# Kernel optimization log

Hardware: AMD Instinct MI355X
Metric: run time of the kernel (lower is better)

## Reference

```python
import jax, jax.numpy as jnp
import numpy as np

BS, HS, NH = 8, 3, 8          # block_size, halo_size, num_heads
WIN = BS + 2 * HS             # 14
DQK = 16                      # dim_head_qk = make_divisible(128*1.0)//8
DV = 16                       # dim_head_v = 128 // 8
SCALE = DQK ** -0.5


def _rel_pos_index():
    # Faithful numpy port of QueryFreePosEmbedRel._get_relative_position_index
    w = WIN
    coords = np.stack(np.meshgrid(np.arange(w), np.arange(w), indexing='ij'))  # (2,w,w)
    flat = coords.reshape(2, -1)                                               # (2, w*w)
    rel = flat[:, :, None] - flat[:, None, :]                                  # (2, ww, ww)
    rel = rel.transpose(1, 2, 0).astype(np.int64)
    rel[:, :, 0] += w - 1
    rel[:, :, 1] += w - 1
    rel[:, :, 0] *= 2 * w - 1
    rel = rel.sum(-1).reshape(w, w, w, w)
    sh = (w - BS) // 2  # == halo_size
    rel = rel[sh:sh + BS, sh:sh + BS, :, :].reshape(BS * BS, w * w)
    return rel

_REL_IDX = _rel_pos_index()


def setup_inputs() -> dict:
    key = jax.random.key(0)
    k1, k2, k3, k4, k5, k6 = jax.random.split(key, 6)
    C = 128
    dim_out_qk = NH * DQK   # 128
    dim_out_v = NH * DV     # 128
    x = jax.random.normal(k1, (4, 128, 128, C), dtype=jnp.float32)
    q_w = jax.random.normal(k2, (dim_out_qk, C), dtype=jnp.float32) * 0.05
    kv_w = jax.random.normal(k3, (dim_out_qk + dim_out_v, C), dtype=jnp.float32) * 0.05
    pos_table = jax.random.normal(k4, ((2 * WIN - 1) * (2 * WIN - 1), NH), dtype=jnp.float32) * 0.02
    proj_w = jax.random.normal(k5, (dim_out_v, dim_out_v), dtype=jnp.float32) * 0.05
    proj_b = jax.random.normal(k6, (dim_out_v,), dtype=jnp.float32) * 0.01
    return {"x": x, "q_w": q_w, "kv_w": kv_w, "pos_table": pos_table,
            "proj_w": proj_w, "proj_b": proj_b}


def reference(x, q_w, kv_w, pos_table, proj_w, proj_b):
    B, H, W, C = x.shape  # H,W divisible by BS -> no padding branch
    nhb, nwb = H // BS, W // BS
    nb = nhb * nwb

    # --- queries: (B,NH,nb,bs^2,DQK), block-partitioned ---
    q = x @ q_w.T
    q = q.reshape(B, nhb, BS, nwb, BS, NH, DQK).transpose(0, 5, 1, 3, 2, 4, 6)
    q = q.reshape(B, NH, nb, BS * BS, DQK)

    # --- kv 1x1 conv + halo padding + overlapping window extraction ---
    kv = x @ kv_w.T                                   # (B,H,W, NH*(DQK+DV))
    kv = jnp.pad(kv, ((0, 0), (HS, HS), (HS, HS), (0, 0)))
    ri = (np.arange(nhb) * BS)[:, None] + np.arange(WIN)[None, :]
    ci = (np.arange(nwb) * BS)[:, None] + np.arange(WIN)[None, :]
    kvw = kv[:, ri]
    kvw = kvw[:, :, :, ci]
    kvw = kvw.transpose(0, 1, 3, 2, 4, 5).reshape(B, nb, WIN * WIN, NH, DQK + DV)
    kvw = kvw.transpose(0, 3, 1, 2, 4)
    k = kvw[..., :DQK]
    v = kvw[..., DQK:]

    bias = pos_table[_REL_IDX.reshape(-1)].reshape(BS * BS, WIN * WIN, NH)
    bias = bias.transpose(2, 0, 1)[None, :, None]

    # --- scores + halo-boundary mask + softmax ---
    attn = jnp.einsum('bhnqd,bhnkd->bhnqk', q * SCALE, k) + bias
    ones = jnp.pad(jnp.ones((H, W), jnp.float32), ((HS, HS), (HS, HS)))
    mw = ones[ri][:, :, ci].transpose(0, 2, 1, 3).reshape(nb, WIN * WIN)
    valid = (mw > 0)[None, None, :, None, :]
    attn = jnp.where(valid, attn, -jnp.finfo(attn.dtype).max)
    attn = jax.nn.softmax(attn, axis=-1)

    # --- weighted sum over V, fold blocks back to (B,H,W,dim_out_v) ---
    out = jnp.einsum('bhnqk,bhnkd->bhnqd', attn, v)   # (B,NH,nb,bs^2,DV)
    out = out.reshape(B, NH, nhb, nwb, BS, BS, DV)
    out = out.transpose(0, 2, 4, 3, 5, 1, 6).reshape(B, H, W, NH * DV)
    return out @ proj_w.T + proj_b
```

## Files before the change

kernel.cpp:

```cpp
#include <hip/hip_runtime.h>
#include <float.h>


typedef float f32x4 __attribute__((ext_vector_type(4)));
typedef short s16x4 __attribute__((ext_vector_type(4)));
typedef short s16x8 __attribute__((ext_vector_type(8)));
typedef unsigned int u32x2 __attribute__((ext_vector_type(2)));
typedef unsigned int u32x4 __attribute__((ext_vector_type(4)));

__device__ inline ushort f2bf(float f) {
    unsigned u = __float_as_uint(f);
    return (ushort)((u + 0x7FFF + ((u >> 16) & 1)) >> 16);
}
__device__ inline float bf2f(ushort h) { return __uint_as_float((unsigned)h << 16); }
__device__ inline unsigned cvtpk(float a, float b) {
    unsigned r;
    asm("v_cvt_pk_bf16_f32 %0, %1, %2" : "=v"(r) : "v"(a), "v"(b));
    return r;
}
#if __has_builtin(__builtin_amdgcn_exp2f)
#define EXP2(x) __builtin_amdgcn_exp2f(x)
#else
#define EXP2(x) exp2f(x)
#endif

__global__ __launch_bounds__(256) void conv_w(
    const float* __restrict__ q_w, const float* __restrict__ kv_w,
    const float* __restrict__ proj_w, ushort* whi, ushort* wlo)
{
    const int g = blockIdx.x * 256 + threadIdx.x;
    const int row = g >> 7, col = g & 127;
    const float v = (row < 128) ? q_w[row * 128 + col]
                  : (row < 384) ? kv_w[(row - 128) * 128 + col]
                                : proj_w[(row - 384) * 128 + col];
    const ushort h = f2bf(v);
    const int off = ((row >> 4) * 2048) + ((col >> 3) * 128) + ((row & 15) * 8) + (col & 7);
    whi[off] = h;
    wlo[off] = f2bf(v - bf2f(h));
}

__global__ __launch_bounds__(256) void gemm_split(
    const float* A,
    const ushort* __restrict__ Whi, const ushort* __restrict__ Wlo,
    int wbase, int ntc, int tok1,
    ushort* qb, ushort* kvb, float* outf, const float* __restrict__ bias)
{
    __shared__ ushort Ah[128 * 128];
    __shared__ ushort Al[128 * 128];

    const int t = threadIdx.x;
    const int row0 = blockIdx.x * 128;
    const int w = t >> 6, l = t & 63;
    const int wm = w >> 1, wn = w & 1;
    const int lr = l & 15, cA = l >> 4;

#pragma unroll
    for (int i = 0; i < 16; ++i) {
        const int idx = t + i * 256;
        const int p = idx >> 5, fc = idx & 31;
        const float4 v = *(const float4*)(A + (size_t)(row0 + p) * 128 + fc * 4);
        const int base = p * 128 + (((fc >> 1) ^ (p & 7)) << 3) + (fc & 1) * 4;
        const unsigned h01 = cvtpk(v.x, v.y), h23 = cvtpk(v.z, v.w);
        *(u32x2*)&Ah[base] = (u32x2){h01, h23};
        const float hx = __uint_as_float(h01 << 16);
        const float hy = __uint_as_float(h01 & 0xFFFF0000u);
        const float hz = __uint_as_float(h23 << 16);
        const float hw = __uint_as_float(h23 & 0xFFFF0000u);
        *(u32x2*)&Al[base] = (u32x2){ cvtpk(v.x - hx, v.y - hy),
                                      cvtpk(v.z - hz, v.w - hw) };
    }
    __syncthreads();

#pragma unroll 1
    for (int nt = 0; nt < ntc; ++nt) {
        f32x4 acc[4][4];
#pragma unroll
        for (int mf = 0; mf < 4; ++mf)
#pragma unroll
            for (int nf = 0; nf < 4; ++nf) acc[mf][nf] = (f32x4){0.f,0.f,0.f,0.f};

#pragma unroll 1
        for (int kk = 0; kk < 4; ++kk) {
            s16x8 wh[4], wl[4];
#pragma unroll
            for (int nf = 0; nf < 4; ++nf) {
                const int rb = (wbase >> 4) + nt * 8 + wn * 4 + nf;
                const size_t off = (size_t)rb * 2048 + (kk * 4 + cA) * 128 + lr * 8;
                wh[nf] = *(const s16x8*)&Whi[off];
                wl[nf] = *(const s16x8*)&Wlo[off];
            }
#pragma unroll
            for (int mf = 0; mf < 4; ++mf) {
                const int p = wm * 64 + mf * 16 + lr;
                const int off = p * 128 + ((((kk << 2) + cA) ^ (p & 7)) << 3);
                const s16x8 xh = *(const s16x8*)&Ah[off];
                const s16x8 xl = *(const s16x8*)&Al[off];
#pragma unroll
                for (int nf = 0; nf < 4; ++nf) {
                    acc[mf][nf] = __builtin_amdgcn_mfma_f32_16x16x32_bf16(
                                      wh[nf], xh, acc[mf][nf], 0, 0, 0);
                    acc[mf][nf] = __builtin_amdgcn_mfma_f32_16x16x32_bf16(
                                      wh[nf], xl, acc[mf][nf], 0, 0, 0);
                    acc[mf][nf] = __builtin_amdgcn_mfma_f32_16x16x32_bf16(
                                      wl[nf], xh, acc[mf][nf], 0, 0, 0);
                }
            }
        }

#pragma unroll
        for (int mf = 0; mf < 4; ++mf) {
            const size_t pix = row0 + wm * 64 + mf * 16 + lr;
#pragma unroll
            for (int nf = 0; nf < 4; ++nf) {
                const int chan = wn * 64 + nf * 16 + cA * 4;
                const f32x4 o = acc[mf][nf];
                if (tok1) {
                    const u32x2 pk = (u32x2){ cvtpk(o[0], o[1]), cvtpk(o[2], o[3]) };
                    if (nt == 0) {
                        const int head = wn * 4 + nf;
                        *(u32x2*)(qb + ((size_t)head << 20) + pix * 16 + (chan & 15)) = pk;
                    } else {
                        const int gchan = (nt - 1) * 128 + chan;
                        const int head = gchan >> 5;
                        *(u32x2*)(kvb + ((size_t)head << 21) + pix * 32 + (gchan & 31)) = pk;
                    }
                } else {
                    const float4 bv = *(const float4*)(bias + chan);
                    f32x4 r = o;
                    r[0] += bv.x; r[1] += bv.y; r[2] += bv.z; r[3] += bv.w;
                    *(f32x4*)(outf + pix * 128 + chan) = r;
                }
            }
        }
    }
}

__global__ __launch_bounds__(256) void halo_attn(
    float* out,
    const ushort* __restrict__ qg,
    const ushort* __restrict__ kvg,
    const float* __restrict__ pos_table)
{
    __shared__ ushort VT[2][16][232];
    __shared__ float  bias_l[648];
    __shared__ int    keyoff[256];
    __shared__ short  koff2[224];

    const int t  = threadIdx.x;
    const int bi = blockIdx.x, head = blockIdx.y, bp = blockIdx.z;
    const int by = bi >> 4, bx = bi & 15;
    const int w  = t >> 6;
    const int lb = w >> 1;
    const int qh = w & 1;
    const int batch = bp * 2 + lb;
    const int l  = t & 63;
    const int lr = l & 15;
    const int cA = l >> 4;

    const char* kvh = (const char*)(kvg + ((size_t)head << 21) + ((size_t)batch << 19));

    if (t < 224) {
        const int wy = t / 14, wx = t - (t / 14) * 14;
        const int py = by * 8 + wy - 3, px = bx * 8 + wx - 3;
        const bool valid = (t < 196) && ((unsigned)py < 128u) && ((unsigned)px < 128u);
        keyoff[t] = valid ? ((py * 128 + px) * 64) : 0;
        koff2[t]  = valid ? (short)(wy * 21 + wx) : (short)(-200);
    } else {
        keyoff[t] = 0;
    }
    for (int i = t; i < 648; i += 256) {
        if (i < 441) {
            const int ry = i / 21, rx = i - ry * 21;
            bias_l[i] = pos_table[((ry + 3) * 27 + rx + 3) * 8 + head] * 1.44269504f;
        } else {
            bias_l[i] = -30000.0f;
        }
    }
    __syncthreads();

    {
        const int l2 = qh * 64 + l;
        if (l2 < 112) {
            const char* base = kvh + 32;
            const char* s0 = base + keyoff[2 * l2];
            const char* s1 = base + keyoff[2 * l2 + 1];
            const s16x8 a0 = *(const s16x8*)s0;
            const s16x8 a1 = *(const s16x8*)(s0 + 16);
            const s16x8 c0 = *(const s16x8*)s1;
            const s16x8 c1 = *(const s16x8*)(s1 + 16);
#pragma unroll
            for (int j = 0; j < 8; ++j) {
                *(unsigned*)&VT[lb][j][2 * l2] =
                    ((unsigned)(ushort)c0[j] << 16) | (ushort)a0[j];
                *(unsigned*)&VT[lb][j + 8][2 * l2] =
                    ((unsigned)(ushort)c1[j] << 16) | (ushort)a1[j];
            }
        }
    }
    __syncthreads();

    const int gbase = ((lr >> 2) << 3) + (lr & 3);
    const ushort* qhp = qg + ((size_t)head << 20);
    s16x8 qf[2];
    float* optr[2];
    int qoff2[2];
#pragma unroll
    for (int j = 0; j < 2; ++j) {
        const int q = (qh * 2 + j) * 16 + lr;
        const int qy = q >> 3, qx = q & 7;
        const size_t pix = ((size_t)(batch * 128 + by * 8 + qy)) * 128 + bx * 8 + qx;
        optr[j] = out + pix * 128 + head * 16 + cA * 4;
        qoff2[j] = (qy + 13) * 21 + (qx + 13);
#pragma unroll
        for (int k = 0; k < 8; ++k) qf[j][k] = 0;
        if (cA < 2)
            qf[j] = *(const s16x8*)(qhp + pix * 16 + cA * 8);
    }

    f32x4 accv[2];
    float sumf[2];
#pragma unroll
    for (int j = 0; j < 2; ++j) {
        accv[j] = (f32x4){0.f, 0.f, 0.f, 0.f};
        sumf[j] = 0.f;
    }

    s16x8 ak0 = *(const s16x8*)(kvh + keyoff[gbase]     + cA * 16);
    s16x8 ak1 = *(const s16x8*)(kvh + keyoff[gbase + 4] + cA * 16);

#pragma unroll 1
    for (int m = 0; m < 7; ++m) {
        const int nx = 32 * (m + 1) + gbase;
        const s16x8 nk0 = *(const s16x8*)(kvh + keyoff[nx]     + cA * 16);
        const s16x8 nk1 = *(const s16x8*)(kvh + keyoff[nx + 4] + cA * 16);

        const int kb = 32 * m + cA * 8;
        const s16x8 kk = *(const s16x8*)&koff2[kb];
        const s16x8 vt = *(const s16x8*)&VT[lb][lr][kb];

#pragma unroll
        for (int j = 0; j < 2; ++j) {
            const f32x4 sf0 = __builtin_amdgcn_mfma_f32_16x16x32_bf16(
                                  ak0, qf[j], (f32x4){0.f, 0.f, 0.f, 0.f}, 0, 0, 0);
            const f32x4 sf1 = __builtin_amdgcn_mfma_f32_16x16x32_bf16(
                                  ak1, qf[j], (f32x4){0.f, 0.f, 0.f, 0.f}, 0, 0, 0);
            float pr0[4], pr1[4];
#pragma unroll
            for (int r = 0; r < 4; ++r)
                pr0[r] = EXP2(fmaf(sf0[r], 0.36067376f, bias_l[qoff2[j] - (int)kk[r]]));
#pragma unroll
            for (int r = 0; r < 4; ++r)
                pr1[r] = EXP2(fmaf(sf1[r], 0.36067376f, bias_l[qoff2[j] - (int)kk[4 + r]]));
            sumf[j] += ((pr0[0] + pr0[1]) + (pr0[2] + pr0[3]))
                     + ((pr1[0] + pr1[1]) + (pr1[2] + pr1[3]));

            const u32x4 pk = (u32x4){ cvtpk(pr0[0], pr0[1]), cvtpk(pr0[2], pr0[3]),
                                      cvtpk(pr1[0], pr1[1]), cvtpk(pr1[2], pr1[3]) };
            const s16x8 pb = *(const s16x8*)&pk;
            accv[j] = __builtin_amdgcn_mfma_f32_16x16x32_bf16(vt, pb, accv[j], 0, 0, 0);
        }
        ak0 = nk0;
        ak1 = nk1;
    }

#pragma unroll
    for (int j = 0; j < 2; ++j) {
        float s = sumf[j];
        s += __shfl_xor(s, 16);
        s += __shfl_xor(s, 32);
        const float inv = 1.0f / s;
        *(f32x4*)optr[j] = accv[j] * inv;
    }
}

extern "C" void kernel_launch(void* const* d_in, const int* in_sizes, int n_in,
                              void* d_out, int out_size, void* d_ws, size_t ws_size,
                              hipStream_t stream) {
    const float* x      = (const float*)d_in[0];
    const float* q_w    = (const float*)d_in[1];
    const float* kv_w   = (const float*)d_in[2];
    const float* pt     = (const float*)d_in[3];
    const float* proj_w = (const float*)d_in[4];
    const float* proj_b = (const float*)d_in[5];
    float* out = (float*)d_out;

    ushort* ykvb = (ushort*)d_ws;
    ushort* qb   = (ushort*)((char*)d_ws + 33554432);
    ushort* whi  = (ushort*)((char*)d_ws + 33554432 + 16777216);
    ushort* wlo  = whi + 65536;

    const dim3 blk(256);
    conv_w<<<dim3(256), blk, 0, stream>>>(q_w, kv_w, proj_w, whi, wlo);
    gemm_split<<<dim3(512), blk, 0, stream>>>(x, whi, wlo, 0, 3, 1,
                                              qb, ykvb, nullptr, nullptr);
    halo_attn<<<dim3(256, 8, 2), blk, 0, stream>>>(out, qb, ykvb, pt);
    gemm_split<<<dim3(512), blk, 0, stream>>>(out, whi, wlo, 384, 1, 0,
                                              nullptr, nullptr, out, proj_b);
}
```

Measured before the change: 94.13 us.

## Compute softmax denominator via MFMA with validity vector and direct bias addressing

Lays out the key window with a stride of 16 instead of 14, so the relative-position bias index becomes an affine pointer that steps back each iteration. This replaces the per-key koff2 lookup and its gather. Invalid keys are no longer masked by a large negative bias. Their V rows are zeroed, and a bf16 ones/zeros validity vector goes through an extra MFMA that yields the masked softmax denominator, replacing the scalar sum and cross-lane shuffles. The cost is one more MFMA per query tile per step, plus exp values that are computed but thrown away for invalid keys; bf16-rounded probabilities in the denominator may also shift accuracy slightly.

```diff
diff --git a/kernel.cpp b/kernel.cpp
--- a/kernel.cpp
+++ b/kernel.cpp
@@ -142,17 +142,17 @@
     const float* __restrict__ pos_table)
 {
     __shared__ ushort VT[2][16][232];
-    __shared__ float  bias_l[648];
+    __shared__ float  bias_l[444];
     __shared__ int    keyoff[256];
-    __shared__ short  koff2[224];
+    __shared__ ushort vbf[232];
 
     const int t  = threadIdx.x;
-    const int bi = blockIdx.x, head = blockIdx.y, bp = blockIdx.z;
+    const int bi = blockIdx.x, head = blockIdx.y, bpair = blockIdx.z;
     const int by = bi >> 4, bx = bi & 15;
     const int w  = t >> 6;
     const int lb = w >> 1;
     const int qh = w & 1;
-    const int batch = bp * 2 + lb;
+    const int batch = bpair * 2 + lb;
     const int l  = t & 63;
     const int lr = l & 15;
     const int cA = l >> 4;
@@ -160,21 +160,22 @@
     const char* kvh = (const char*)(kvg + ((size_t)head << 21) + ((size_t)batch << 19));
 
     if (t < 224) {
-        const int wy = t / 14, wx = t - (t / 14) * 14;
+        const int wy = t >> 4, wx = t & 15;
         const int py = by * 8 + wy - 3, px = bx * 8 + wx - 3;
-        const bool valid = (t < 196) && ((unsigned)py < 128u) && ((unsigned)px < 128u);
+        const bool valid = (wx < 14) && ((unsigned)py < 128u) && ((unsigned)px < 128u);
         keyoff[t] = valid ? ((py * 128 + px) * 64) : 0;
-        koff2[t]  = valid ? (short)(wy * 21 + wx) : (short)(-200);
+        vbf[t]    = valid ? (ushort)0x3F80 : (ushort)0;
     } else {
         keyoff[t] = 0;
-    }
-    for (int i = t; i < 648; i += 256) {
-        if (i < 441) {
-            const int ry = i / 21, rx = i - ry * 21;
-            bias_l[i] = pos_table[((ry + 3) * 27 + rx + 3) * 8 + head] * 1.44269504f;
-        } else {
-            bias_l[i] = -30000.0f;
-        }
+        if (t < 232) vbf[t] = 0;
+    }
+    for (int i = t; i < 444; i += 256) {
+        float v = 0.f;
+        if (i >= 2) {
+            const int r = i - 2, ry = r / 21, rx = r - ry * 21;
+            v = pos_table[((ry + 3) * 27 + rx + 3) * 8 + head] * 1.44269504f;
+        }
+        bias_l[i] = v;
     }
     __syncthreads();
 
@@ -182,12 +183,15 @@
         const int l2 = qh * 64 + l;
         if (l2 < 112) {
             const char* base = kvh + 32;
+            const bool v0 = vbf[2 * l2] != 0;
+            const bool v1 = vbf[2 * l2 + 1] != 0;
+            const s16x8 z = (s16x8){0,0,0,0,0,0,0,0};
             const char* s0 = base + keyoff[2 * l2];
             const char* s1 = base + keyoff[2 * l2 + 1];
-            const s16x8 a0 = *(const s16x8*)s0;
-            const s16x8 a1 = *(const s16x8*)(s0 + 16);
-            const s16x8 c0 = *(const s16x8*)s1;
-            const s16x8 c1 = *(const s16x8*)(s1 + 16);
+            const s16x8 a0 = v0 ? *(const s16x8*)s0 : z;
+            const s16x8 a1 = v0 ? *(const s16x8*)(s0 + 16) : z;
+            const s16x8 c0 = v1 ? *(const s16x8*)s1 : z;
+            const s16x8 c1 = v1 ? *(const s16x8*)(s1 + 16) : z;
 #pragma unroll
             for (int j = 0; j < 8; ++j) {
                 *(unsigned*)&VT[lb][j][2 * l2] =
@@ -201,28 +205,28 @@
 
     const int gbase = ((lr >> 2) << 3) + (lr & 3);
     const ushort* qhp = qg + ((size_t)head << 20);
+    const int wy0 = cA >> 1, wx0 = (cA & 1) * 8;
     s16x8 qf[2];
     float* optr[2];
-    int qoff2[2];
+    const float* bptr[2];
 #pragma unroll
     for (int j = 0; j < 2; ++j) {
         const int q = (qh * 2 + j) * 16 + lr;
         const int qy = q >> 3, qx = q & 7;
         const size_t pix = ((size_t)(batch * 128 + by * 8 + qy)) * 128 + bx * 8 + qx;
         optr[j] = out + pix * 128 + head * 16 + cA * 4;
-        qoff2[j] = (qy + 13) * 21 + (qx + 13);
+        bptr[j] = bias_l + 2 + (qy + 13 - wy0) * 21 + (qx + 6 - wx0);
 #pragma unroll
         for (int k = 0; k < 8; ++k) qf[j][k] = 0;
         if (cA < 2)
             qf[j] = *(const s16x8*)(qhp + pix * 16 + cA * 8);
     }
 
-    f32x4 accv[2];
-    float sumf[2];
+    f32x4 accv[2], accs[2];
 #pragma unroll
     for (int j = 0; j < 2; ++j) {
         accv[j] = (f32x4){0.f, 0.f, 0.f, 0.f};
-        sumf[j] = 0.f;
+        accs[j] = (f32x4){0.f, 0.f, 0.f, 0.f};
     }
 
     s16x8 ak0 = *(const s16x8*)(kvh + keyoff[gbase]     + cA * 16);
@@ -235,8 +239,8 @@
         const s16x8 nk1 = *(const s16x8*)(kvh + keyoff[nx + 4] + cA * 16);
 
         const int kb = 32 * m + cA * 8;
-        const s16x8 kk = *(const s16x8*)&koff2[kb];
-        const s16x8 vt = *(const s16x8*)&VT[lb][lr][kb];
+        const s16x8 vt  = *(const s16x8*)&VT[lb][lr][kb];
+        const s16x8 vld = *(const s16x8*)&vbf[kb];
 
 #pragma unroll
         for (int j = 0; j < 2; ++j) {
@@ -244,31 +248,30 @@
                                   ak0, qf[j], (f32x4){0.f, 0.f, 0.f, 0.f}, 0, 0, 0);
             const f32x4 sf1 = __builtin_amdgcn_mfma_f32_16x16x32_bf16(
                                   ak1, qf[j], (f32x4){0.f, 0.f, 0.f, 0.f}, 0, 0, 0);
+            const float* bq = bptr[j];
             float pr0[4], pr1[4];
 #pragma unroll
             for (int r = 0; r < 4; ++r)
-                pr0[r] = EXP2(fmaf(sf0[r], 0.36067376f, bias_l[qoff2[j] - (int)kk[r]]));
+                pr0[r] = EXP2(fmaf(sf0[r], 0.36067376f, bq[7 - r]));
 #pragma unroll
             for (int r = 0; r < 4; ++r)
-                pr1[r] = EXP2(fmaf(sf1[r], 0.36067376f, bias_l[qoff2[j] - (int)kk[4 + r]]));
-            sumf[j] += ((pr0[0] + pr0[1]) + (pr0[2] + pr0[3]))
-                     + ((pr1[0] + pr1[1]) + (pr1[2] + pr1[3]));
+                pr1[r] = EXP2(fmaf(sf1[r], 0.36067376f, bq[3 - r]));
 
             const u32x4 pk = (u32x4){ cvtpk(pr0[0], pr0[1]), cvtpk(pr0[2], pr0[3]),
                                       cvtpk(pr1[0], pr1[1]), cvtpk(pr1[2], pr1[3]) };
             const s16x8 pb = *(const s16x8*)&pk;
-            accv[j] = __builtin_amdgcn_mfma_f32_16x16x32_bf16(vt, pb, accv[j], 0, 0, 0);
-        }
+            accv[j] = __builtin_amdgcn_mfma_f32_16x16x32_bf16(vt,  pb, accv[j], 0, 0, 0);
+            accs[j] = __builtin_amdgcn_mfma_f32_16x16x32_bf16(vld, pb, accs[j], 0, 0, 0);
+        }
+        bptr[0] -= 42;
+        bptr[1] -= 42;
         ak0 = nk0;
         ak1 = nk1;
     }
 
 #pragma unroll
     for (int j = 0; j < 2; ++j) {
-        float s = sumf[j];
-        s += __shfl_xor(s, 16);
-        s += __shfl_xor(s, 32);
-        const float inv = 1.0f / s;
+        const float inv = 1.0f / accs[j][0];
         *(f32x4*)optr[j] = accv[j] * inv;
     }
 }
```

Measured after the change: 117.6 us. 1.25x slower.
